# Kernel tuning notes

Measured on AMD Instinct MI355X. Metric: run time of the kernel, lower is better.

Reference implementation:

```python
import jax, jax.numpy as jnp
import numpy as np

B, N, D, E, H = 4, 2048, 512, 16, 1024
CAP = max(4, min(N, int(N * 2.0 / E)))   # eval capacity_factor = 2.0 -> 256
EPS = 1e-9
THRESH = 0.2  # second_threshold_eval


def setup_inputs() -> dict:
    key = jax.random.key(0)
    ks = jax.random.split(key, 10)
    f32 = jnp.float32
    return {
        "X": jax.random.normal(ks[0], (B, N, D), f32),
        "probs": jax.random.uniform(ks[1], (B, N), f32),
        "W1": jax.random.normal(ks[2], (D, D), f32) * (1.0 / np.sqrt(D)),
        "b1": jnp.zeros((D,), f32),
        "Wg": jax.random.normal(ks[3], (D, E), f32),  # Top2Gating uses randn init
        "We1": jax.random.normal(ks[4], (E, D, H), f32) * (1.0 / np.sqrt(D)),
        "We2": jax.random.normal(ks[5], (E, H, D), f32) * (1.0 / np.sqrt(H)),
        "W3": jax.random.normal(ks[6], (D, 4), f32) * (1.0 / np.sqrt(D)),
        "b3": jnp.zeros((4,), f32),
        "W4": jax.random.normal(ks[7], (4, 1), f32) * 0.5,
        "b4": jnp.zeros((1,), f32),
    }


def top2_gating(x, Wg, probs):
    # x: [B, N, D] -> raw gates [B, N, E]
    raw = jax.nn.softmax(jnp.einsum('bnd,de->bne', x, Wg), axis=-1)
    dt = raw.dtype

    gate1 = jnp.max(raw, axis=-1)
    idx1 = jnp.argmax(raw, axis=-1)
    mask1 = jax.nn.one_hot(idx1, E, dtype=dt)
    density_proxy = raw

    raw_wo1 = raw * (1.0 - mask1)
    gate2 = jnp.max(raw_wo1, axis=-1)
    idx2 = jnp.argmax(raw_wo1, axis=-1)
    mask2 = jax.nn.one_hot(idx2, E, dtype=dt)

    denom = gate1 + gate2 + EPS
    gate1 = gate1 / denom
    gate2 = gate2 / denom

    # load-balancing loss (computed but wrapper discards it)
    density1 = jnp.mean(mask1, axis=-2)
    loss = jnp.mean(jnp.mean(density_proxy, axis=-2) * density1) * float(E ** 2)

    # second policy == 'random'
    mask2 = mask2 * (probs < (gate2 / max(THRESH, EPS))).astype(dt)[..., None]

    # exclusive cumsum along the group dim gives position within each expert
    pos1 = (jnp.cumsum(mask1, axis=-2) - mask1) * mask1          # [B, N, E]
    mask1 = mask1 * (pos1 < float(CAP)).astype(dt)
    mask1_count = jnp.sum(mask1, axis=-2, keepdims=True)
    mask1_flat = jnp.sum(mask1, axis=-1)                          # [B, N]
    pos1_flat = jnp.sum(pos1, axis=-1)
    gate1 = gate1 * mask1_flat

    pos2 = ((jnp.cumsum(mask2, axis=-2) - mask2) + mask1_count) * mask2
    mask2 = mask2 * (pos2 < float(CAP)).astype(dt)
    mask2_flat = jnp.sum(mask2, axis=-1)
    pos2_flat = jnp.sum(pos2, axis=-1)
    gate2 = gate2 * mask2_flat

    # safe one-hot: out-of-range positions map to all-zeros (jax.nn.one_hot semantics)
    oh_p1 = jax.nn.one_hot(pos1_flat.astype(jnp.int32), CAP, dtype=dt)
    oh_p2 = jax.nn.one_hot(pos2_flat.astype(jnp.int32), CAP, dtype=dt)
    oh_e1 = jax.nn.one_hot(idx1, E, dtype=dt)
    oh_e2 = jax.nn.one_hot(idx2, E, dtype=dt)

    combine = ((gate1 * mask1_flat)[..., None, None] * oh_e1[..., :, None] * oh_p1[..., None, :]
               + (gate2 * mask2_flat)[..., None, None] * oh_e2[..., :, None] * oh_p2[..., None, :])
    dispatch = (combine != 0).astype(dt)
    return dispatch, combine, loss


def reference(X, probs, W1, b1, Wg, We1, We2, W3, b3, W4, b4):
    h = X @ W1 + b1                                              # linear1
    dispatch, combine, loss = top2_gating(h, Wg, probs)
    exp_in = jnp.einsum('bnd,bnec->ebcd', h, dispatch)           # dispatch
    hid = jax.nn.leaky_relu(jnp.einsum('ebcd,edh->ebch', exp_in, We1))
    exp_out = jnp.einsum('ebch,ehd->ebcd', hid, We2)             # experts
    moe_out = jnp.einsum('bnec,ebcd->bnd', combine, exp_out)     # combine
    out = (moe_out @ W3 + b3) @ W4 + b4                          # hidden3 -> act3
    return out
```

## Files before the change

### kernel.cpp

```cpp
#include <hip/hip_runtime.h>
#include <hip/hip_bf16.h>

#define NB 4
#define NN 2048
#define ND 512
#define NE 16
#define NH 1024
#define CAP 256
#define NTOK (NB*NN)

typedef __attribute__((ext_vector_type(8))) short bf16x8;
typedef __attribute__((ext_vector_type(4))) float f32x4;
typedef __attribute__((ext_vector_type(8))) unsigned short u16x8;

__device__ __forceinline__ void gload16(const void* gsrc, void* lds) {
    __builtin_amdgcn_global_load_lds((const __attribute__((address_space(1))) void*)gsrc,
                                     (__attribute__((address_space(3))) void*)lds, 16, 0, 0);
}
__device__ __forceinline__ unsigned short f2bf(float f) {
    union { __hip_bfloat16 b; unsigned short u; } v; v.b = __float2bfloat16(f); return v.u;
}

__global__ __launch_bounds__(256) void prep_w_kernel(const float* __restrict__ W1,
                                                     const float* __restrict__ Wg,
                                                     unsigned short* __restrict__ W1B,
                                                     float* __restrict__ WcT,
                                                     float* __restrict__ zbuf) {
    const int tid = threadIdx.x;
    int bid = blockIdx.x;
    if (bid < 128) {
        if (bid == 0) zbuf[tid] = 0.f;
        const int w = tid >> 6, l = tid & 63;
        const int d = bid * 4 + w;
        float a0 = 0.f, a1 = 0.f, a2 = 0.f, a3 = 0.f, a4 = 0.f, a5 = 0.f, a6 = 0.f, a7 = 0.f;
        float a8 = 0.f, a9 = 0.f, aA = 0.f, aB = 0.f, aC = 0.f, aD = 0.f, aE = 0.f, aF = 0.f;
        #pragma unroll
        for (int ch = 0; ch < 8; ++ch) {
            float x = W1[(size_t)d * ND + ch * 64 + l];
            const float4* wg4 = (const float4*)(Wg + (size_t)(ch * 64 + l) * NE);
            float4 g0 = wg4[0], g1 = wg4[1], g2 = wg4[2], g3 = wg4[3];
            a0 = fmaf(x, g0.x, a0); a1 = fmaf(x, g0.y, a1); a2 = fmaf(x, g0.z, a2); a3 = fmaf(x, g0.w, a3);
            a4 = fmaf(x, g1.x, a4); a5 = fmaf(x, g1.y, a5); a6 = fmaf(x, g1.z, a6); a7 = fmaf(x, g1.w, a7);
            a8 = fmaf(x, g2.x, a8); a9 = fmaf(x, g2.y, a9); aA = fmaf(x, g2.z, aA); aB = fmaf(x, g2.w, aB);
            aC = fmaf(x, g3.x, aC); aD = fmaf(x, g3.y, aD); aE = fmaf(x, g3.z, aE); aF = fmaf(x, g3.w, aF);
        }
        float accs[16] = {a0, a1, a2, a3, a4, a5, a6, a7, a8, a9, aA, aB, aC, aD, aE, aF};
        #pragma unroll
        for (int off = 32; off >= 1; off >>= 1)
            #pragma unroll
            for (int e = 0; e < 16; ++e) accs[e] += __shfl_xor(accs[e], off);
        #pragma unroll
        for (int e = 0; e < 16; ++e)
            if (l == e) WcT[e * ND + d] = accs[e];
        return;
    }
    bid -= 128;
    {
        int dblk = bid >> 1, hblk = bid & 1;
        const float* src = W1 + (size_t)(dblk * 64) * ND + hblk * 256 + tid;
        unsigned short* dst = W1B + (size_t)(dblk * 512 + hblk * 256 + tid) * 64;
        float v[64];
        #pragma unroll
        for (int j = 0; j < 64; ++j) v[j] = src[(size_t)j * ND];
        #pragma unroll
        for (int q = 0; q < 8; ++q) {
            u16x8 o;
            #pragma unroll
            for (int j = 0; j < 8; ++j) o[j] = f2bf(v[q * 8 + j]);
            *(u16x8*)(dst + q * 8) = o;
        }
    }
}

__global__ __launch_bounds__(256) void gating_kernel(const float* __restrict__ X,
                                                     const float* __restrict__ WcT,
                                                     const float* __restrict__ probs,
                                                     const float* __restrict__ b3,
                                                     const float* __restrict__ W4,
                                                     const float* __restrict__ b4,
                                                     unsigned short* __restrict__ Xbf,
                                                     int* __restrict__ idx1a, int* __restrict__ idx2a,
                                                     float* __restrict__ g1a, float* __restrict__ g2a,
                                                     float* __restrict__ out) {
    __shared__ float wc[NE * ND];
    const int tid = threadIdx.x;
    const int bid = blockIdx.x;
    const int w = tid >> 6, l = tid & 63;
    #pragma unroll
    for (int i = 0; i < 32; ++i) wc[tid + 256 * i] = WcT[tid + 256 * i];
    float c0v = b4[0];
    #pragma unroll
    for (int j = 0; j < 4; ++j) c0v += b3[j] * W4[j];
    __syncthreads();
    const float4* wc4 = (const float4*)wc;
    for (int j = 0; j < 4; ++j) {
        int tok = bid * 16 + j * 4 + w;
        const float4* xrow = (const float4*)(X + (size_t)tok * ND);
        float4 x0 = xrow[l], x1 = xrow[l + 64];
        {
            ushort4 o0, o1;
            o0.x = f2bf(x0.x); o0.y = f2bf(x0.y); o0.z = f2bf(x0.z); o0.w = f2bf(x0.w);
            o1.x = f2bf(x1.x); o1.y = f2bf(x1.y); o1.z = f2bf(x1.z); o1.w = f2bf(x1.w);
            *(ushort4*)(Xbf + (size_t)tok * ND + 4 * l) = o0;
            *(ushort4*)(Xbf + (size_t)tok * ND + 256 + 4 * l) = o1;
        }
        float acc[NE];
        #pragma unroll
        for (int e = 0; e < NE; ++e) {
            float4 w0 = wc4[e * 128 + l], w1 = wc4[e * 128 + l + 64];
            acc[e] = x0.x * w0.x + x0.y * w0.y + x0.z * w0.z + x0.w * w0.w
                   + x1.x * w1.x + x1.y * w1.y + x1.z * w1.z + x1.w * w1.w;
        }
        #pragma unroll
        for (int off = 32; off >= 1; off >>= 1)
            #pragma unroll
            for (int e = 0; e < NE; ++e) acc[e] += __shfl_xor(acc[e], off);

        if (l == 0) {
            float m = acc[0];
            #pragma unroll
            for (int e = 1; e < NE; ++e) m = fmaxf(m, acc[e]);
            float s = 0.f;
            #pragma unroll
            for (int e = 0; e < NE; ++e) { acc[e] = expf(acc[e] - m); s += acc[e]; }
            float inv = 1.f / s;
            #pragma unroll
            for (int e = 0; e < NE; ++e) acc[e] *= inv;
            int i1 = 0; float g1 = acc[0];
            #pragma unroll
            for (int e = 1; e < NE; ++e) if (acc[e] > g1) { g1 = acc[e]; i1 = e; }
            int i2 = -1; float g2 = -1.f;
            #pragma unroll
            for (int e = 0; e < NE; ++e) if (e != i1 && acc[e] > g2) { g2 = acc[e]; i2 = e; }
            float denom = g1 + g2 + 1e-9f;
            float g1n = g1 / denom, g2n = g2 / denom;
            bool flag = probs[tok] < (g2n / 0.2f);
            idx1a[tok] = i1;
            idx2a[tok] = flag ? i2 : -1;
            g1a[tok] = g1n;
            g2a[tok] = g2n;
            out[tok] = c0v;
        }
    }
}

__global__ __launch_bounds__(512) void post_kernel(const int* __restrict__ idx1a,
                                                   const int* __restrict__ idx2a,
                                                   int* __restrict__ slot_token,
                                                   const unsigned short* __restrict__ Xbf,
                                                   const unsigned short* __restrict__ W1B,
                                                   const float* __restrict__ b1,
                                                   unsigned short* __restrict__ hbf,
                                                   const float* __restrict__ We1,
                                                   unsigned short* __restrict__ We1B,
                                                   const float* __restrict__ We2,
                                                   const float* __restrict__ W3,
                                                   const float* __restrict__ W4,
                                                   float* __restrict__ u) {
    __shared__ char smem[32768];
    const int tid = threadIdx.x;
    const int w = tid >> 6, l = tid & 63;
    if (blockIdx.x < 64) {
        const int bb = blockIdx.x;
        const int b = bb >> 4, e = bb & 15;
        int* cnt1 = (int*)smem;
        int* cnt2 = cnt1 + 8;
        int* slot = slot_token + (e * NB + b) * CAP;
        const unsigned long long below = (l == 0) ? 0ull : ((1ull << l) - 1ull);
        const int base0 = w * 256;
        int c1 = 0, c2 = 0;
        #pragma unroll
        for (int it = 0; it < 4; ++it) {
            int n = base0 + it * 64 + l;
            c1 += __popcll(__ballot(idx1a[b * NN + n] == e));
            c2 += __popcll(__ballot(idx2a[b * NN + n] == e));
        }
        if (l == 0) { cnt1[w] = c1; cnt2[w] = c2; }
        __syncthreads();
        int b1c = 0, t1 = 0, b2c = 0, t2 = 0;
        #pragma unroll
        for (int i = 0; i < 8; ++i) {
            int v1 = cnt1[i], v2 = cnt2[i];
            if (i < w) { b1c += v1; b2c += v2; }
            t1 += v1; t2 += v2;
        }
        const int start2 = (t1 < CAP) ? t1 : CAP;
        int c = b1c;
        #pragma unroll
        for (int it = 0; it < 4; ++it) {
            int n = base0 + it * 64 + l;
            bool p = (idx1a[b * NN + n] == e);
            unsigned long long m = __ballot(p);
            int pre = __popcll(m & below);
            if (p) { int pos = c + pre; if (pos < CAP) slot[pos] = n; }
            c += __popcll(m);
        }
        c = start2 + b2c;
        #pragma unroll
        for (int it = 0; it < 4; ++it) {
            int n = base0 + it * 64 + l;
            bool p = (idx2a[b * NN + n] == e);
            unsigned long long m = __ballot(p);
            int pre = __popcll(m & below);
            if (p) { int pos = c + pre; if (pos < CAP) slot[pos] = n | (1 << 30); }
            c += __popcll(m);
        }
        int nfill = start2 + t2; nfill = (nfill < CAP) ? nfill : CAP;
        for (int i = nfill + tid; i < CAP; i += 512) slot[i] = -1;
        return;
    }
    if (blockIdx.x < 320) {
        const int lb = blockIdx.x - 64;
        const int m0 = (lb >> 2) * 128, n0 = (lb & 3) * 128;
        const int wm = w >> 1, wn = w & 1;
        const int lr = l & 15, lk = l >> 4;
        char* Ash0 = smem;
        char* Bsh0 = smem + 16384;

        f32x4 acc[2][4] = {};
        for (int Ks = 0; Ks < 8; ++Ks) {
            __syncthreads();
            {
                int o = tid * 16;
                int r0 = o >> 7, bb = o & 127;
                int sb2 = bb ^ ((r0 & 7) << 4);
                gload16((const char*)Xbf + ((size_t)(m0 + r0) * ND + Ks * 64) * 2 + sb2,
                        Ash0 + o);
                int o2 = o + 8192;
                int r1 = o2 >> 7;
                int sb3 = bb ^ ((r1 & 7) << 4);
                gload16((const char*)Xbf + ((size_t)(m0 + r1) * ND + Ks * 64) * 2 + sb3,
                        Ash0 + o2);
                gload16((const char*)W1B + ((size_t)(Ks * 512 + n0 + r0) * 64) * 2 + sb2,
                        Bsh0 + o);
                gload16((const char*)W1B + ((size_t)(Ks * 512 + n0 + r1) * 64) * 2 + sb3,
                        Bsh0 + o2);
            }
            __syncthreads();
            #pragma unroll
            for (int k32 = 0; k32 < 2; ++k32) {
                int kb = (k32 * 32 + 8 * lk) * 2;
                bf16x8 a[2], bfr[4];
                #pragma unroll
                for (int mi = 0; mi < 2; ++mi) {
                    int row = wm * 32 + mi * 16 + lr;
                    a[mi] = *(const bf16x8*)(Ash0 + row * 128 + (kb ^ ((row & 7) << 4)));
                }
                #pragma unroll
                for (int ni = 0; ni < 4; ++ni) {
                    int row = wn * 64 + ni * 16 + lr;
                    bfr[ni] = *(const bf16x8*)(Bsh0 + row * 128 + (kb ^ ((row & 7) << 4)));
                }
                #pragma unroll
                for (int mi = 0; mi < 2; ++mi)
                    #pragma unroll
                    for (int ni = 0; ni < 4; ++ni)
                        acc[mi][ni] = __builtin_amdgcn_mfma_f32_16x16x32_bf16(a[mi], bfr[ni], acc[mi][ni], 0, 0, 0);
            }
        }
        #pragma unroll
        for (int mi = 0; mi < 2; ++mi)
            #pragma unroll
            for (int ni = 0; ni < 4; ++ni) {
                int col = n0 + wn * 64 + ni * 16 + lr;
                float bb1 = b1[col];
                #pragma unroll
                for (int r = 0; r < 4; ++r) {
                    int m = m0 + wm * 32 + mi * 16 + lk * 4 + r;
                    hbf[(size_t)m * ND + col] = f2bf(acc[mi][ni][r] + bb1);
                }
            }
        return;
    }
    if (blockIdx.x < 832) {
        const int unit = blockIdx.x - 320;
        const int e = unit >> 5, rem = unit & 31;
        const int dblk = rem >> 2, hq = rem & 3;
        const int dhalf = tid >> 8, hl = tid & 255;
        const float* src = We1 + (size_t)e * ND * NH + (size_t)(dblk * 64 + dhalf * 32) * NH + hq * 256 + hl;
        unsigned short* dst = We1B + ((size_t)(e * 8 + dblk) * NH + hq * 256 + hl) * 64 + dhalf * 32;
        float v[32];
        #pragma unroll
        for (int j = 0; j < 32; ++j) v[j] = src[(size_t)j * NH];
        #pragma unroll
        for (int q = 0; q < 4; ++q) {
            u16x8 o;
            #pragma unroll
            for (int j = 0; j < 8; ++j) o[j] = f2bf(v[q * 8 + j]);
            *(u16x8*)(dst + q * 8) = o;
        }
        return;
    }
    {
        const int ub = blockIdx.x - 832;
        float* vvs = (float*)smem;
        {
            float s0 = 0.f;
            #pragma unroll
            for (int j = 0; j < 4; ++j) s0 += W3[tid * 4 + j] * W4[j];
            vvs[tid] = s0;
        }
        __syncthreads();
        const float4* vv4 = (const float4*)vvs;
        const float4 v0 = vv4[l], v1 = vv4[l + 64];
        #pragma unroll
        for (int pass = 0; pass < 4; ++pass) {
            float sums[8];
            #pragma unroll
            for (int i = 0; i < 8; ++i) {
                int gr = ub * 256 + pass * 64 + w * 8 + i;
                const float4* row = (const float4*)(We2 + (size_t)gr * ND);
                float4 a0 = row[l], a1 = row[l + 64];
                sums[i] = a0.x * v0.x + a0.y * v0.y + a0.z * v0.z + a0.w * v0.w
                        + a1.x * v1.x + a1.y * v1.y + a1.z * v1.z + a1.w * v1.w;
            }
            #pragma unroll
            for (int off = 32; off >= 1; off >>= 1)
                #pragma unroll
                for (int i = 0; i < 8; ++i) sums[i] += __shfl_xor(sums[i], off);
            if (l == 0) {
                int gr0 = ub * 256 + pass * 64 + w * 8;
                #pragma unroll
                for (int i = 0; i < 8; ++i) u[gr0 + i] = sums[i];
            }
        }
    }
}

__global__ __launch_bounds__(512) void expert_mfma_kernel(const unsigned short* __restrict__ hbf,
                                                          const unsigned short* __restrict__ We1B,
                                                          const float* __restrict__ u,
                                                          const int* __restrict__ slot_token,
                                                          const float* __restrict__ zbuf,
                                                          const float* __restrict__ g1a,
                                                          const float* __restrict__ g2a,
                                                          float* __restrict__ out) {
    __shared__ char Ash[65536];
    __shared__ char Bsh[2][32768];
    __shared__ float u_lds[NH];
    __shared__ float sbuf[8][64];
    __shared__ int toks[64];
    const int tid = threadIdx.x;
    const int w = tid >> 6, l = tid & 63;
    const int lr = l & 15, lk = l >> 4;
    const int bid = blockIdx.x;
    const int e = (bid & 7) | ((bid >> 7) << 3);
    const int chunk = (bid >> 3) & 15;
    const int b = chunk >> 2, c0 = (chunk & 3) * 64;

    if (tid < 64) toks[tid] = slot_token[(e * NB + b) * CAP + c0 + tid];
    u_lds[tid] = u[e * NH + tid];
    u_lds[tid + 512] = u[e * NH + tid + 512];
    __syncthreads();
    #pragma unroll
    for (int i = 0; i < 8; ++i) {
        int r = i * 8 + w;
        int t = toks[r];
        int tok = t & 2047;
        int sb = (l * 16) ^ ((r & 7) << 4);
        const char* src = (t >= 0) ? ((const char*)hbf + ((size_t)(b * NN + tok) * ND) * 2 + sb)
                                   : ((const char*)zbuf + sb);
        gload16(src, Ash + i * 8192 + w * 1024);
    }
    auto stageB = [&](int s, int buf) {
        int Hc = s >> 4, Ks = s & 15;
        const size_t base = ((size_t)(e * 8 + (Ks >> 1)) * NH + Hc * 512) * 64 + (Ks & 1) * 32;
        #pragma unroll
        for (int i = 0; i < 4; ++i) {
            int r = i * 128 + w * 16 + (l >> 2);
            int swzr = ((r >> 1) & 3) << 4;
            int ebyte = ((l & 3) * 16) ^ swzr;
            gload16((const char*)We1B + (base + (size_t)r * 64) * 2 + ebyte,
                    Bsh[buf] + i * 8192 + w * 1024);
        }
    };
    f32x4 acc[4][4] = {};
    float srow[4][4] = {};
    stageB(0, 0);
    __syncthreads();
    for (int s = 0; s < 32; ++s) {
        int buf = s & 1;
        if (s < 31) stageB(s + 1, buf ^ 1);
        int Ks = s & 15;
        bf16x8 a[4], bb[4];
        #pragma unroll
        for (int mi = 0; mi < 4; ++mi) {
            int row = mi * 16 + lr;
            int kb = (Ks * 64 + lk * 16) ^ ((row & 7) << 4);
            a[mi] = *(const bf16x8*)(Ash + row * 1024 + kb);
        }
        #pragma unroll
        for (int ni = 0; ni < 4; ++ni) {
            int row = w * 64 + ni * 16 + lr;
            int kb = (lk * 16) ^ (((row >> 1) & 3) << 4);
            bb[ni] = *(const bf16x8*)(Bsh[buf] + row * 64 + kb);
        }
        #pragma unroll
        for (int mi = 0; mi < 4; ++mi)
            #pragma unroll
            for (int ni = 0; ni < 4; ++ni)
                acc[mi][ni] = __builtin_amdgcn_mfma_f32_16x16x32_bf16(a[mi], bb[ni], acc[mi][ni], 0, 0, 0);
        if ((s & 15) == 15) {
            int Hc = s >> 4;
            #pragma unroll
            for (int ni = 0; ni < 4; ++ni) {
                float uu = u_lds[Hc * 512 + w * 64 + ni * 16 + lr];
                #pragma unroll
                for (int mi = 0; mi < 4; ++mi)
                    #pragma unroll
                    for (int r = 0; r < 4; ++r) {
                        float x = acc[mi][ni][r];
                        x = (x > 0.f) ? x : 0.01f * x;
                        srow[mi][r] = fmaf(x, uu, srow[mi][r]);
                        acc[mi][ni][r] = 0.f;
                    }
            }
        }
        __syncthreads();
    }
    #pragma unroll
    for (int off = 1; off < 16; off <<= 1)
        #pragma unroll
        for (int mi = 0; mi < 4; ++mi)
            #pragma unroll
            for (int r = 0; r < 4; ++r)
                srow[mi][r] += __shfl_xor(srow[mi][r], off);
    if (lr == 0) {
        #pragma unroll
        for (int mi = 0; mi < 4; ++mi)
            #pragma unroll
            for (int r = 0; r < 4; ++r)
                sbuf[w][mi * 16 + lk * 4 + r] = srow[mi][r];
    }
    __syncthreads();
    if (tid < 64) {
        float s = 0.f;
        #pragma unroll
        for (int q = 0; q < 8; ++q) s += sbuf[q][tid];
        int v = toks[tid];
        if (v >= 0) {
            int tok = v & 2047;
            float g = (v & (1 << 30)) ? g2a[b * NN + tok] : g1a[b * NN + tok];
            atomicAdd(out + b * NN + tok, s * g);
        }
    }
}

extern "C" void kernel_launch(void* const* d_in, const int* in_sizes, int n_in,
                              void* d_out, int out_size, void* d_ws, size_t ws_size,
                              hipStream_t stream) {
    const float* X    = (const float*)d_in[0];
    const float* probs= (const float*)d_in[1];
    const float* W1   = (const float*)d_in[2];
    const float* b1   = (const float*)d_in[3];
    const float* Wg   = (const float*)d_in[4];
    const float* We1  = (const float*)d_in[5];
    const float* We2  = (const float*)d_in[6];
    const float* W3   = (const float*)d_in[7];
    const float* b3   = (const float*)d_in[8];
    const float* W4   = (const float*)d_in[9];
    const float* b4   = (const float*)d_in[10];
    float* out = (float*)d_out;

    char* ws = (char*)d_ws;
    size_t off = 0;
    auto alloc = [&](size_t bytes) { void* p = ws + off; off += (bytes + 255) & ~(size_t)255; return p; };
    unsigned short* Xbf  = (unsigned short*)alloc((size_t)NTOK * ND * 2);
    unsigned short* hbf  = (unsigned short*)alloc((size_t)NTOK * ND * 2);
    unsigned short* W1B  = (unsigned short*)alloc((size_t)ND * ND * 2);
    unsigned short* We1B = (unsigned short*)alloc((size_t)NE * NH * ND * 2);
    float* WcT     = (float*)alloc(NE * ND * 4);
    float* u       = (float*)alloc(NE * NH * 4);
    float* zbuf    = (float*)alloc(1024);
    int*   idx1a   = (int*)alloc(NTOK * 4);
    int*   idx2a   = (int*)alloc(NTOK * 4);
    float* g1a     = (float*)alloc(NTOK * 4);
    float* g2a     = (float*)alloc(NTOK * 4);
    int*   slot_tok= (int*)alloc(NE * NB * CAP * 4);
    (void)ws_size; (void)in_sizes; (void)n_in; (void)out_size;

    prep_w_kernel<<<144, 256, 0, stream>>>(W1, Wg, W1B, WcT, zbuf);
    gating_kernel<<<512, 256, 0, stream>>>(X, WcT, probs, b3, W4, b4, Xbf,
                                           idx1a, idx2a, g1a, g2a, out);
    post_kernel<<<896, 512, 0, stream>>>(idx1a, idx2a, slot_tok,
                                         Xbf, W1B, b1, hbf,
                                         We1, We1B, We2, W3, W4, u);
    expert_mfma_kernel<<<256, 512, 0, stream>>>(hbf, We1B, u, slot_tok, zbuf, g1a, g2a, out);
}
```

Baseline: 81.47 us.

## Fuse prep, gating and post kernels into one persistent kernel with atomic counters

Merges the three pre-expert kernels into a single launch. Dependent stages are ordered with global atomic counters that blocks spin-wait on (release/acquire with threadfence). The aim is to remove launch gaps and let independent work (We1 conversion, We2 reduction) overlap the dependent stages. It adds a memset launch and relies on the producer blocks (lower block ids) being scheduled before the waiting consumers, which risks deadlock or stalls if scheduling order differs.

```diff
diff --git a/kernel.cpp b/kernel.cpp
--- a/kernel.cpp
+++ b/kernel.cpp
@@ -20,18 +20,39 @@
 __device__ __forceinline__ unsigned short f2bf(float f) {
     union { __hip_bfloat16 b; unsigned short u; } v; v.b = __float2bfloat16(f); return v.u;
 }
-
-__global__ __launch_bounds__(256) void prep_w_kernel(const float* __restrict__ W1,
-                                                     const float* __restrict__ Wg,
-                                                     unsigned short* __restrict__ W1B,
-                                                     float* __restrict__ WcT,
-                                                     float* __restrict__ zbuf) {
+__device__ __forceinline__ void block_release(int* c) {
+    __threadfence();
+    __syncthreads();
+    if (threadIdx.x == 0) atomicAdd(c, 1);
+}
+__device__ __forceinline__ void block_acquire(int* c, int target) {
+    if (threadIdx.x == 0)
+        while (atomicAdd(c, 0) < target) __builtin_amdgcn_s_sleep(2);
+    __syncthreads();
+    __threadfence();
+}
+
+__global__ __launch_bounds__(512) void mega1_kernel(
+        const float* __restrict__ X, const float* __restrict__ probs,
+        const float* __restrict__ W1, const float* __restrict__ b1,
+        const float* __restrict__ Wg, const float* __restrict__ We1,
+        const float* __restrict__ We2, const float* __restrict__ W3,
+        const float* __restrict__ b3, const float* __restrict__ W4,
+        const float* __restrict__ b4,
+        unsigned short* __restrict__ Xbf, unsigned short* __restrict__ hbf,
+        unsigned short* __restrict__ W1B, unsigned short* __restrict__ We1B,
+        float* __restrict__ WcT, float* __restrict__ u, float* __restrict__ zbuf,
+        int* __restrict__ idx1a, int* __restrict__ idx2a,
+        float* __restrict__ g1a, float* __restrict__ g2a,
+        int* __restrict__ slot_token, float* __restrict__ out,
+        int* __restrict__ ctr) {
+    __shared__ __align__(16) char smem[32768];
     const int tid = threadIdx.x;
-    int bid = blockIdx.x;
-    if (bid < 128) {
-        if (bid == 0) zbuf[tid] = 0.f;
-        const int w = tid >> 6, l = tid & 63;
-        const int d = bid * 4 + w;
+    const int bid = blockIdx.x;
+    const int w = tid >> 6, l = tid & 63;
+    if (bid < 64) {
+        if (bid == 0 && tid < 256) zbuf[tid] = 0.f;
+        const int d = bid * 8 + w;
         float a0 = 0.f, a1 = 0.f, a2 = 0.f, a3 = 0.f, a4 = 0.f, a5 = 0.f, a6 = 0.f, a7 = 0.f;
         float a8 = 0.f, a9 = 0.f, aA = 0.f, aB = 0.f, aC = 0.f, aD = 0.f, aE = 0.f, aF = 0.f;
         #pragma unroll
@@ -52,116 +73,94 @@
         #pragma unroll
         for (int e = 0; e < 16; ++e)
             if (l == e) WcT[e * ND + d] = accs[e];
-        return;
-    }
-    bid -= 128;
-    {
-        int dblk = bid >> 1, hblk = bid & 1;
-        const float* src = W1 + (size_t)(dblk * 64) * ND + hblk * 256 + tid;
-        unsigned short* dst = W1B + (size_t)(dblk * 512 + hblk * 256 + tid) * 64;
-        float v[64];
-        #pragma unroll
-        for (int j = 0; j < 64; ++j) v[j] = src[(size_t)j * ND];
-        #pragma unroll
-        for (int q = 0; q < 8; ++q) {
-            u16x8 o;
-            #pragma unroll
-            for (int j = 0; j < 8; ++j) o[j] = f2bf(v[q * 8 + j]);
-            *(u16x8*)(dst + q * 8) = o;
-        }
-    }
-}
-
-__global__ __launch_bounds__(256) void gating_kernel(const float* __restrict__ X,
-                                                     const float* __restrict__ WcT,
-                                                     const float* __restrict__ probs,
-                                                     const float* __restrict__ b3,
-                                                     const float* __restrict__ W4,
-                                                     const float* __restrict__ b4,
-                                                     unsigned short* __restrict__ Xbf,
-                                                     int* __restrict__ idx1a, int* __restrict__ idx2a,
-                                                     float* __restrict__ g1a, float* __restrict__ g2a,
-                                                     float* __restrict__ out) {
-    __shared__ float wc[NE * ND];
-    const int tid = threadIdx.x;
-    const int bid = blockIdx.x;
-    const int w = tid >> 6, l = tid & 63;
-    #pragma unroll
-    for (int i = 0; i < 32; ++i) wc[tid + 256 * i] = WcT[tid + 256 * i];
-    float c0v = b4[0];
-    #pragma unroll
-    for (int j = 0; j < 4; ++j) c0v += b3[j] * W4[j];
-    __syncthreads();
-    const float4* wc4 = (const float4*)wc;
-    for (int j = 0; j < 4; ++j) {
-        int tok = bid * 16 + j * 4 + w;
-        const float4* xrow = (const float4*)(X + (size_t)tok * ND);
-        float4 x0 = xrow[l], x1 = xrow[l + 64];
-        {
-            ushort4 o0, o1;
-            o0.x = f2bf(x0.x); o0.y = f2bf(x0.y); o0.z = f2bf(x0.z); o0.w = f2bf(x0.w);
-            o1.x = f2bf(x1.x); o1.y = f2bf(x1.y); o1.z = f2bf(x1.z); o1.w = f2bf(x1.w);
-            *(ushort4*)(Xbf + (size_t)tok * ND + 4 * l) = o0;
-            *(ushort4*)(Xbf + (size_t)tok * ND + 256 + 4 * l) = o1;
-        }
-        float acc[NE];
-        #pragma unroll
-        for (int e = 0; e < NE; ++e) {
-            float4 w0 = wc4[e * 128 + l], w1 = wc4[e * 128 + l + 64];
-            acc[e] = x0.x * w0.x + x0.y * w0.y + x0.z * w0.z + x0.w * w0.w
-                   + x1.x * w1.x + x1.y * w1.y + x1.z * w1.z + x1.w * w1.w;
-        }
-        #pragma unroll
-        for (int off = 32; off >= 1; off >>= 1)
-            #pragma unroll
-            for (int e = 0; e < NE; ++e) acc[e] += __shfl_xor(acc[e], off);
-
-        if (l == 0) {
-            float m = acc[0];
-            #pragma unroll
-            for (int e = 1; e < NE; ++e) m = fmaxf(m, acc[e]);
-            float s = 0.f;
-            #pragma unroll
-            for (int e = 0; e < NE; ++e) { acc[e] = expf(acc[e] - m); s += acc[e]; }
-            float inv = 1.f / s;
-            #pragma unroll
-            for (int e = 0; e < NE; ++e) acc[e] *= inv;
-            int i1 = 0; float g1 = acc[0];
-            #pragma unroll
-            for (int e = 1; e < NE; ++e) if (acc[e] > g1) { g1 = acc[e]; i1 = e; }
-            int i2 = -1; float g2 = -1.f;
-            #pragma unroll
-            for (int e = 0; e < NE; ++e) if (e != i1 && acc[e] > g2) { g2 = acc[e]; i2 = e; }
-            float denom = g1 + g2 + 1e-9f;
-            float g1n = g1 / denom, g2n = g2 / denom;
-            bool flag = probs[tok] < (g2n / 0.2f);
-            idx1a[tok] = i1;
-            idx2a[tok] = flag ? i2 : -1;
-            g1a[tok] = g1n;
-            g2a[tok] = g2n;
-            out[tok] = c0v;
-        }
-    }
-}
-
-__global__ __launch_bounds__(512) void post_kernel(const int* __restrict__ idx1a,
-                                                   const int* __restrict__ idx2a,
-                                                   int* __restrict__ slot_token,
-                                                   const unsigned short* __restrict__ Xbf,
-                                                   const unsigned short* __restrict__ W1B,
-                                                   const float* __restrict__ b1,
-                                                   unsigned short* __restrict__ hbf,
-                                                   const float* __restrict__ We1,
-                                                   unsigned short* __restrict__ We1B,
-                                                   const float* __restrict__ We2,
-                                                   const float* __restrict__ W3,
-                                                   const float* __restrict__ W4,
-                                                   float* __restrict__ u) {
-    __shared__ char smem[32768];
-    const int tid = threadIdx.x;
-    const int w = tid >> 6, l = tid & 63;
-    if (blockIdx.x < 64) {
-        const int bb = blockIdx.x;
+        block_release(ctr + 0);
+        return;
+    }
+    if (bid < 72) {
+        const int dblk = bid - 64;
+        const float* src = W1 + (size_t)(dblk * 64) * ND + tid;
+        unsigned short* dst = W1B + (size_t)(dblk * 512 + tid) * 64;
+        #pragma unroll
+        for (int half = 0; half < 2; ++half) {
+            float v[32];
+            #pragma unroll
+            for (int j = 0; j < 32; ++j) v[j] = src[(size_t)(half * 32 + j) * ND];
+            #pragma unroll
+            for (int q = 0; q < 4; ++q) {
+                u16x8 o;
+                #pragma unroll
+                for (int j = 0; j < 8; ++j) o[j] = f2bf(v[q * 8 + j]);
+                *(u16x8*)(dst + half * 32 + q * 8) = o;
+            }
+        }
+        block_release(ctr + 0);
+        return;
+    }
+    if (bid < 328) {
+        block_acquire(ctr + 0, 72);
+        const int gb = bid - 72;
+        float* wc = (float*)smem;
+        #pragma unroll
+        for (int i = 0; i < 16; ++i) wc[tid + 512 * i] = WcT[tid + 512 * i];
+        float c0v = b4[0];
+        #pragma unroll
+        for (int j = 0; j < 4; ++j) c0v += b3[j] * W4[j];
+        __syncthreads();
+        const float4* wc4 = (const float4*)wc;
+        for (int j = 0; j < 4; ++j) {
+            int tok = gb * 32 + j * 8 + w;
+            const float4* xrow = (const float4*)(X + (size_t)tok * ND);
+            float4 x0 = xrow[l], x1 = xrow[l + 64];
+            {
+                ushort4 o0, o1;
+                o0.x = f2bf(x0.x); o0.y = f2bf(x0.y); o0.z = f2bf(x0.z); o0.w = f2bf(x0.w);
+                o1.x = f2bf(x1.x); o1.y = f2bf(x1.y); o1.z = f2bf(x1.z); o1.w = f2bf(x1.w);
+                *(ushort4*)(Xbf + (size_t)tok * ND + 4 * l) = o0;
+                *(ushort4*)(Xbf + (size_t)tok * ND + 256 + 4 * l) = o1;
+            }
+            float acc[NE];
+            #pragma unroll
+            for (int e = 0; e < NE; ++e) {
+                float4 w0 = wc4[e * 128 + l], w1 = wc4[e * 128 + l + 64];
+                acc[e] = x0.x * w0.x + x0.y * w0.y + x0.z * w0.z + x0.w * w0.w
+                       + x1.x * w1.x + x1.y * w1.y + x1.z * w1.z + x1.w * w1.w;
+            }
+            #pragma unroll
+            for (int off = 32; off >= 1; off >>= 1)
+                #pragma unroll
+                for (int e = 0; e < NE; ++e) acc[e] += __shfl_xor(acc[e], off);
+            if (l == 0) {
+                float m = acc[0];
+                #pragma unroll
+                for (int e = 1; e < NE; ++e) m = fmaxf(m, acc[e]);
+                float s = 0.f;
+                #pragma unroll
+                for (int e = 0; e < NE; ++e) { acc[e] = expf(acc[e] - m); s += acc[e]; }
+                float inv = 1.f / s;
+                #pragma unroll
+                for (int e = 0; e < NE; ++e) acc[e] *= inv;
+                int i1 = 0; float g1 = acc[0];
+                #pragma unroll
+                for (int e = 1; e < NE; ++e) if (acc[e] > g1) { g1 = acc[e]; i1 = e; }
+                int i2 = -1; float g2 = -1.f;
+                #pragma unroll
+                for (int e = 0; e < NE; ++e) if (e != i1 && acc[e] > g2) { g2 = acc[e]; i2 = e; }
+                float denom = g1 + g2 + 1e-9f;
+                float g1n = g1 / denom, g2n = g2 / denom;
+                bool flag = probs[tok] < (g2n / 0.2f);
+                idx1a[tok] = i1;
+                idx2a[tok] = flag ? i2 : -1;
+                g1a[tok] = g1n;
+                g2a[tok] = g2n;
+                out[tok] = c0v;
+            }
+        }
+        block_release(ctr + 1);
+        return;
+    }
+    if (bid < 392) {
+        block_acquire(ctr + 1, 256);
+        const int bb = bid - 328;
         const int b = bb >> 4, e = bb & 15;
         int* cnt1 = (int*)smem;
         int* cnt2 = cnt1 + 8;
@@ -209,14 +208,14 @@
         for (int i = nfill + tid; i < CAP; i += 512) slot[i] = -1;
         return;
     }
-    if (blockIdx.x < 320) {
-        const int lb = blockIdx.x - 64;
+    if (bid < 648) {
+        block_acquire(ctr + 1, 256);
+        const int lb = bid - 392;
         const int m0 = (lb >> 2) * 128, n0 = (lb & 3) * 128;
         const int wm = w >> 1, wn = w & 1;
         const int lr = l & 15, lk = l >> 4;
         char* Ash0 = smem;
         char* Bsh0 = smem + 16384;
-
         f32x4 acc[2][4] = {};
         for (int Ks = 0; Ks < 8; ++Ks) {
             __syncthreads();
@@ -224,17 +223,13 @@
                 int o = tid * 16;
                 int r0 = o >> 7, bb = o & 127;
                 int sb2 = bb ^ ((r0 & 7) << 4);
-                gload16((const char*)Xbf + ((size_t)(m0 + r0) * ND + Ks * 64) * 2 + sb2,
-                        Ash0 + o);
+                gload16((const char*)Xbf + ((size_t)(m0 + r0) * ND + Ks * 64) * 2 + sb2, Ash0 + o);
                 int o2 = o + 8192;
                 int r1 = o2 >> 7;
                 int sb3 = bb ^ ((r1 & 7) << 4);
-                gload16((const char*)Xbf + ((size_t)(m0 + r1) * ND + Ks * 64) * 2 + sb3,
-                        Ash0 + o2);
-                gload16((const char*)W1B + ((size_t)(Ks * 512 + n0 + r0) * 64) * 2 + sb2,
-                        Bsh0 + o);
-                gload16((const char*)W1B + ((size_t)(Ks * 512 + n0 + r1) * 64) * 2 + sb3,
-                        Bsh0 + o2);
+                gload16((const char*)Xbf + ((size_t)(m0 + r1) * ND + Ks * 64) * 2 + sb3, Ash0 + o2);
+                gload16((const char*)W1B + ((size_t)(Ks * 512 + n0 + r0) * 64) * 2 + sb2, Bsh0 + o);
+                gload16((const char*)W1B + ((size_t)(Ks * 512 + n0 + r1) * 64) * 2 + sb3, Bsh0 + o2);
             }
             __syncthreads();
             #pragma unroll
@@ -272,8 +267,8 @@
             }
         return;
     }
-    if (blockIdx.x < 832) {
-        const int unit = blockIdx.x - 320;
+    if (bid < 1160) {
+        const int unit = bid - 648;
         const int e = unit >> 5, rem = unit & 31;
         const int dblk = rem >> 2, hq = rem & 3;
         const int dhalf = tid >> 8, hl = tid & 255;
@@ -292,7 +287,7 @@
         return;
     }
     {
-        const int ub = blockIdx.x - 832;
+        const int ub = bid - 1160;
         float* vvs = (float*)smem;
         {
             float s0 = 0.f;
@@ -477,13 +472,12 @@
     float* g1a     = (float*)alloc(NTOK * 4);
     float* g2a     = (float*)alloc(NTOK * 4);
     int*   slot_tok= (int*)alloc(NE * NB * CAP * 4);
+    int*   ctr     = (int*)alloc(256);
     (void)ws_size; (void)in_sizes; (void)n_in; (void)out_size;
 
-    prep_w_kernel<<<144, 256, 0, stream>>>(W1, Wg, W1B, WcT, zbuf);
-    gating_kernel<<<512, 256, 0, stream>>>(X, WcT, probs, b3, W4, b4, Xbf,
-                                           idx1a, idx2a, g1a, g2a, out);
-    post_kernel<<<896, 512, 0, stream>>>(idx1a, idx2a, slot_tok,
-                                         Xbf, W1B, b1, hbf,
-                                         We1, We1B, We2, W3, W4, u);
+    hipMemsetAsync(ctr, 0, 256, stream);
+    mega1_kernel<<<1224, 512, 0, stream>>>(X, probs, W1, b1, Wg, We1, We2, W3, b3, W4, b4,
+                                           Xbf, hbf, W1B, We1B, WcT, u, zbuf,
+                                           idx1a, idx2a, g1a, g2a, slot_tok, out, ctr);
     expert_mfma_kernel<<<256, 512, 0, stream>>>(hbf, We1B, u, slot_tok, zbuf, g1a, g2a, out);
 }
```

Result: slower. 213.1 us (+161.5%).
